# Optimization experiments

Measured on AMD Instinct MI355X. Metric: run time of the kernel, lower is better.

Reference implementation:

```python
import jax, jax.numpy as jnp
import numpy as np

N_NODES = 100000
N_EDGES = 1600000
HIDDEN = 128
N_GRAPHS = 64
N_CLASSES = 10


def setup_inputs() -> dict:
    key = jax.random.key(0)
    ks = jax.random.split(key, 10)
    x = jax.random.normal(ks[0], (N_NODES, 1), dtype=jnp.float32)
    edge_index = jax.random.randint(ks[1], (2, N_EDGES), 0, N_NODES, dtype=jnp.int32)
    batch = jnp.sort(jax.random.randint(ks[2], (N_NODES,), 0, N_GRAPHS, dtype=jnp.int32))
    def glorot(k, shape):
        fan_in, fan_out = shape
        s = jnp.sqrt(6.0 / (fan_in + fan_out))
        return jax.random.uniform(k, shape, jnp.float32, -s, s)
    return {
        "x": x,
        "edge_index": edge_index,
        "batch": batch,
        "W1l": glorot(ks[3], (1, HIDDEN)),
        "W1r": glorot(ks[4], (1, HIDDEN)),
        "b1": jnp.zeros((HIDDEN,), jnp.float32),
        "W2l": glorot(ks[5], (HIDDEN, HIDDEN)),
        "W2r": glorot(ks[6], (HIDDEN, HIDDEN)),
        "b2": jnp.zeros((HIDDEN,), jnp.float32),
        "W3l": glorot(ks[7], (HIDDEN, HIDDEN)),
        "W3r": glorot(ks[8], (HIDDEN, HIDDEN)),
        "b3": jnp.zeros((HIDDEN,), jnp.float32),
        "Wfc": glorot(ks[9], (HIDDEN, N_CLASSES)),
        "bfc": jnp.zeros((N_CLASSES,), jnp.float32),
    }


def _sage_conv(x, src, dst, Wl, Wr, b, n_nodes):
    # mean aggregation of source features at destination nodes
    msg = x[src]                                              # [E, d_in]
    agg = jax.ops.segment_sum(msg, dst, num_segments=n_nodes)  # [N, d_in]
    cnt = jax.ops.segment_sum(jnp.ones((src.shape[0], 1), x.dtype), dst,
                              num_segments=n_nodes)            # [N, 1]
    mean = agg / jnp.maximum(cnt, 1.0)
    # PyG SAGEConv: lin_l(mean neighbors) + bias + lin_r(self)
    return mean @ Wl + b + x @ Wr


def reference(x, edge_index, batch, W1l, W1r, b1, W2l, W2r, b2,
              W3l, W3r, b3, Wfc, bfc):
    src, dst = edge_index[0], edge_index[1]
    n = x.shape[0]
    h = jax.nn.relu(_sage_conv(x, src, dst, W1l, W1r, b1, n))
    h = jax.nn.relu(_sage_conv(h, src, dst, W2l, W2r, b2, n))
    h = jax.nn.relu(_sage_conv(h, src, dst, W3l, W3r, b3, n))
    # global_mean_pool over graph ids in `batch`
    pooled = jax.ops.segment_sum(h, batch, num_segments=N_GRAPHS)
    gcnt = jax.ops.segment_sum(jnp.ones((n, 1), h.dtype), batch,
                               num_segments=N_GRAPHS)
    pooled = pooled / jnp.maximum(gcnt, 1.0)
    logits = pooled @ Wfc + bfc
    return jax.nn.log_softmax(logits, axis=1)
```

## Files before the change

kernel.cpp:

```cpp
#include <hip/hip_runtime.h>

typedef unsigned int u32;
typedef unsigned short u16;
typedef short bf16x8 __attribute__((ext_vector_type(8)));
typedef float f32x4 __attribute__((ext_vector_type(4)));
typedef float f32x2 __attribute__((ext_vector_type(2)));
typedef u32 u32x4 __attribute__((ext_vector_type(4)));

#define HBLK 256

__device__ __forceinline__ u16 f2bf(float f) {
  u32 u = __float_as_uint(f);
  u = (u + 0x7FFFu + ((u >> 16) & 1u)) >> 16;
  return (u16)u;
}
__device__ __forceinline__ float bf2f(u32 h) { return __uint_as_float(h << 16); }

__global__ void hist_kernel(const int* __restrict__ dst, int* __restrict__ hist,
                            int E, int nbuk, int chunk) {
  __shared__ int h[1024];
  for (int i = threadIdx.x; i < nbuk; i += 256) h[i] = 0;
  __syncthreads();
  int b0 = blockIdx.x * chunk, b1 = min(b0 + chunk, E);
  for (int e = b0 + threadIdx.x; e < b1; e += 256)
    atomicAdd(&h[dst[e] >> 7], 1);
  __syncthreads();
  for (int i = threadIdx.x; i < nbuk; i += 256)
    hist[i * HBLK + blockIdx.x] = h[i];
}

__global__ void scan_local(const int* __restrict__ in, int* __restrict__ out,
                           int* __restrict__ bsum, int n) {
  __shared__ int s[256];
  int tid = threadIdx.x;
  int i = blockIdx.x * 256 + tid;
  int v = (i < n) ? in[i] : 0;
  s[tid] = v;
  __syncthreads();
  for (int off = 1; off < 256; off <<= 1) {
    int t = (tid >= off) ? s[tid - off] : 0;
    __syncthreads();
    s[tid] += t;
    __syncthreads();
  }
  if (i < n) out[i] = s[tid] - v;
  if (tid == 255) bsum[blockIdx.x] = s[255];
}

__global__ void scan_fix(int* __restrict__ a, const int* __restrict__ bsum, int n) {
  __shared__ int red[256];
  int tid = threadIdx.x, b = blockIdx.x;
  int s = 0;
  for (int k = tid; k < b; k += 256) s += bsum[k];
  red[tid] = s;
  __syncthreads();
  for (int off = 128; off; off >>= 1) {
    if (tid < off) red[tid] += red[tid + off];
    __syncthreads();
  }
  int i = b * 256 + tid;
  if (i < n) a[i] += red[0];
}

__global__ void scatter2_kernel(const int* __restrict__ src, const int* __restrict__ dst,
                                const int* __restrict__ hist_s, u32* __restrict__ part,
                                int E, int nbuk, int chunk) {
  __shared__ int cur[1024];
  for (int i = threadIdx.x; i < nbuk; i += 256)
    cur[i] = hist_s[i * HBLK + blockIdx.x];
  __syncthreads();
  int b0 = blockIdx.x * chunk, b1 = min(b0 + chunk, E);
  for (int e = b0 + threadIdx.x; e < b1; e += 256) {
    int d = dst[e];
    int pos = atomicAdd(&cur[d >> 7], 1);
    part[pos] = (u32)src[e] | ((u32)(d & 127) << 25);
  }
}

__global__ void scatter3_kernel(const u32* __restrict__ part, const int* __restrict__ hist_s,
                                const float* __restrict__ x,
                                int* __restrict__ roff, int* __restrict__ csr,
                                float* __restrict__ mean1, int E, int nbuk, int n) {
  int b = blockIdx.x;
  int tid = threadIdx.x;
  int base = hist_s[b * HBLK];
  int end = (b + 1 < nbuk) ? hist_s[(b + 1) * HBLK] : E;
  __shared__ int cnt[128];
  __shared__ int s[128];
  __shared__ int cur[128];
  __shared__ float xsum[128];
  if (tid < 128) { cnt[tid] = 0; xsum[tid] = 0.f; }
  __syncthreads();
  for (int e = base + tid; e < end; e += 256)
    atomicAdd(&cnt[part[e] >> 25], 1);
  __syncthreads();
  if (tid < 128) s[tid] = cnt[tid];
  __syncthreads();
  for (int off = 1; off < 128; off <<= 1) {
    int t = (tid >= off && tid < 128) ? s[tid - off] : 0;
    __syncthreads();
    if (tid < 128) s[tid] += t;
    __syncthreads();
  }
  if (tid < 128) {
    int excl = s[tid] - cnt[tid];
    cur[tid] = base + excl;
    int node = b * 128 + tid;
    if (node < n) roff[node] = base + excl;
  }
  if (b == 0 && tid == 0) roff[n] = E;
  __syncthreads();
  for (int e = base + tid; e < end; e += 256) {
    u32 p = part[e];
    int sidx = (int)(p & 0x1FFFFFFu);
    int pos = atomicAdd(&cur[p >> 25], 1);
    csr[pos] = sidx;
    atomicAdd(&xsum[p >> 25], x[sidx]);
  }
  __syncthreads();
  if (tid < 128) {
    int node = b * 128 + tid;
    if (node < n) mean1[node] = xsum[tid] / (float)max(cnt[tid], 1);
  }
}

__global__ void h1_kernel(const float* __restrict__ mean1, const float* __restrict__ x,
                          const float* __restrict__ W1l, const float* __restrict__ W1r,
                          const float* __restrict__ b1, u32* __restrict__ h1, int n) {
  int idx = blockIdx.x * 256 + threadIdx.x;
  if (idx >= n * 64) return;
  int i = idx >> 6, w = idx & 63;
  int j0 = w * 2;
  float m1 = mean1[i], xs = x[i];
  float v0 = fmaxf(m1 * W1l[j0] + xs * W1r[j0] + b1[j0], 0.f);
  float v1 = fmaxf(m1 * W1l[j0 + 1] + xs * W1r[j0 + 1] + b1[j0 + 1], 0.f);
  h1[idx] = (u32)f2bf(v0) | ((u32)f2bf(v1) << 16);
}

__global__ void wprep2_kernel(const float* __restrict__ W2l, const float* __restrict__ W2r,
                              const float* __restrict__ W3l, const float* __restrict__ W3r,
                              u16* __restrict__ wt2, u16* __restrict__ wt3,
                              float* __restrict__ pooled, int* __restrict__ gcnt) {
  int idx = blockIdx.x * 256 + threadIdx.x;
  int which = idx >> 15, r = idx & 32767;
  int j = r >> 8, k = r & 255;
  if (which == 0) {
    float v = (k < 128) ? W2l[k * 128 + j] : W2r[(k - 128) * 128 + j];
    wt2[r] = f2bf(v);
  } else {
    float v = (k < 128) ? W3l[k * 128 + j] : W3r[(k - 128) * 128 + j];
    wt3[r] = f2bf(v);
  }
  if (idx < 8192) pooled[idx] = 0.f;
  if (idx < 64) gcnt[idx] = 0;
}

__global__ void agg_kernel(const int* __restrict__ csr, const int* __restrict__ roff,
                           const u32* __restrict__ hin, u32* __restrict__ outv, int n) {
  int wave = threadIdx.x >> 6, lane = threadIdx.x & 63;
  int i = blockIdx.x * 4 + wave;
  if (i >= n) return;
  int grp = lane >> 4, li = lane & 15;
  int e0 = roff[i], e1 = roff[i + 1];
  f32x2 a[4] = {};
  int e = e0 + grp;
  for (; e + 12 < e1; e += 16) {
    int s0 = csr[e], s1 = csr[e + 4], s2 = csr[e + 8], s3 = csr[e + 12];
    u32x4 v0 = *(const u32x4*)(hin + (size_t)s0 * 64 + li * 4);
    u32x4 v1 = *(const u32x4*)(hin + (size_t)s1 * 64 + li * 4);
    u32x4 v2 = *(const u32x4*)(hin + (size_t)s2 * 64 + li * 4);
    u32x4 v3 = *(const u32x4*)(hin + (size_t)s3 * 64 + li * 4);
#pragma unroll
    for (int w = 0; w < 4; ++w) {
      a[w] += (f32x2){bf2f(v0[w] & 0xFFFFu), bf2f(v0[w] >> 16)};
      a[w] += (f32x2){bf2f(v1[w] & 0xFFFFu), bf2f(v1[w] >> 16)};
      a[w] += (f32x2){bf2f(v2[w] & 0xFFFFu), bf2f(v2[w] >> 16)};
      a[w] += (f32x2){bf2f(v3[w] & 0xFFFFu), bf2f(v3[w] >> 16)};
    }
  }
  for (; e + 4 < e1; e += 8) {
    int s0 = csr[e], s1 = csr[e + 4];
    u32x4 v0 = *(const u32x4*)(hin + (size_t)s0 * 64 + li * 4);
    u32x4 v1 = *(const u32x4*)(hin + (size_t)s1 * 64 + li * 4);
#pragma unroll
    for (int w = 0; w < 4; ++w) {
      a[w] += (f32x2){bf2f(v0[w] & 0xFFFFu), bf2f(v0[w] >> 16)};
      a[w] += (f32x2){bf2f(v1[w] & 0xFFFFu), bf2f(v1[w] >> 16)};
    }
  }
  if (e < e1) {
    int s0 = csr[e];
    u32x4 v0 = *(const u32x4*)(hin + (size_t)s0 * 64 + li * 4);
#pragma unroll
    for (int w = 0; w < 4; ++w)
      a[w] += (f32x2){bf2f(v0[w] & 0xFFFFu), bf2f(v0[w] >> 16)};
  }
#pragma unroll
  for (int w = 0; w < 4; ++w) {
    a[w].x += __shfl_xor(a[w].x, 16, 64);
    a[w].y += __shfl_xor(a[w].y, 16, 64);
    a[w].x += __shfl_xor(a[w].x, 32, 64);
    a[w].y += __shfl_xor(a[w].y, 32, 64);
  }
  if (grp == 0) {
    float inv = 1.f / (float)max(e1 - e0, 1);
    u32x4 o;
#pragma unroll
    for (int w = 0; w < 4; ++w)
      o[w] = (u32)f2bf(a[w].x * inv) | ((u32)f2bf(a[w].y * inv) << 16);
    *(u32x4*)(outv + (size_t)i * 64 + li * 4) = o;
  }
}

__launch_bounds__(512)
__global__ void mm_kernel(const u16* Aleft, const u16* Aright,
                          const u16* __restrict__ Wt, const float* __restrict__ bias,
                          u16* Out, int n) {
  __shared__ u16 wlds[32768];
  for (int c = threadIdx.x; c < 4096; c += 512) {
    int j = c >> 5, ch = c & 31;
    int swz = ch ^ (j & 31);
    *(u32x4*)(&wlds[j * 256 + swz * 8]) = *(const u32x4*)(&Wt[j * 256 + ch * 8]);
  }
  __syncthreads();
  int wave = threadIdx.x >> 6;
  int lane = threadIdx.x & 63;
  int quad = lane >> 4, l16 = lane & 15;
  int row0 = blockIdx.x * 128 + wave * 16;
  int m = row0 + l16;
  int mc = m < n ? m : (n - 1);
  f32x4 acc[8] = {};
  const u16* Ah[2] = {Aleft, Aright};
#pragma unroll
  for (int half = 0; half < 2; ++half) {
    const u16* A = Ah[half] + (size_t)mc * 128;
#pragma unroll
    for (int s = 0; s < 4; ++s) {
      bf16x8 a = *(const bf16x8*)(A + s * 32 + quad * 8);
      int chunk = (half << 4) + (s << 2) + quad;
#pragma unroll
      for (int t = 0; t < 8; ++t) {
        int j = t * 16 + l16;
        int swz = chunk ^ (j & 31);
        bf16x8 b = *(const bf16x8*)(&wlds[j * 256 + swz * 8]);
        acc[t] = __builtin_amdgcn_mfma_f32_16x16x32_bf16(a, b, acc[t], 0, 0, 0);
      }
    }
  }
#pragma unroll
  for (int t = 0; t < 8; ++t) {
    int j = t * 16 + l16;
    float bj = bias[j];
#pragma unroll
    for (int r = 0; r < 4; ++r) {
      int mr = row0 + quad * 4 + r;
      if (mr < n) {
        float v = acc[t][r] + bj;
        Out[(size_t)mr * 128 + j] = f2bf(fmaxf(v, 0.f));
      }
    }
  }
}

#define PB_NODES 256
__global__ void pool_partial(const int* __restrict__ batch, const u32* __restrict__ h3,
                             float* __restrict__ pooled, int* __restrict__ gcnt, int n) {
  int wave = threadIdx.x >> 6, lane = threadIdx.x & 63;
  int start = blockIdx.x * PB_NODES;
  int end = min(start + PB_NODES, n);
  float a0 = 0.f, a1 = 0.f;
  int gcur = -1, cnt = 0;
  for (int i = start + wave; i < end; i += 4) {
    int g = batch[i];
    if (g != gcur) {
      if (gcur >= 0) {
        atomicAdd(&pooled[gcur * 128 + lane * 2], a0);
        atomicAdd(&pooled[gcur * 128 + lane * 2 + 1], a1);
        if (lane == 0) atomicAdd(&gcnt[gcur], cnt);
      }
      gcur = g; a0 = 0.f; a1 = 0.f; cnt = 0;
    }
    u32 v = h3[(size_t)i * 64 + lane];
    a0 += bf2f(v & 0xFFFFu);
    a1 += bf2f(v >> 16);
    cnt++;
  }
  if (gcur >= 0) {
    atomicAdd(&pooled[gcur * 128 + lane * 2], a0);
    atomicAdd(&pooled[gcur * 128 + lane * 2 + 1], a1);
    if (lane == 0) atomicAdd(&gcnt[gcur], cnt);
  }
}

__global__ void head_kernel(const float* __restrict__ pooled, const int* __restrict__ gcnt,
                            const float* __restrict__ Wfc, const float* __restrict__ bfc,
                            float* __restrict__ out) {
  __shared__ float lg[64][10];
  int t = threadIdx.x;
  if (t < 640) {
    int g = t / 10, c = t % 10;
    float inv = 1.f / (float)max(gcnt[g], 1);
    float acc = bfc[c];
    for (int k = 0; k < 128; ++k) acc += pooled[g * 128 + k] * inv * Wfc[k * 10 + c];
    lg[g][c] = acc;
  }
  __syncthreads();
  if (t < 640) {
    int g = t / 10, c = t % 10;
    float mx = -1e30f;
    for (int q = 0; q < 10; ++q) mx = fmaxf(mx, lg[g][q]);
    float se = 0.f;
    for (int q = 0; q < 10; ++q) se += expf(lg[g][q] - mx);
    out[g * 10 + c] = lg[g][c] - mx - logf(se);
  }
}

extern "C" void kernel_launch(void* const* d_in, const int* in_sizes, int n_in,
                              void* d_out, int out_size, void* d_ws, size_t ws_size,
                              hipStream_t stream) {
  const float* x   = (const float*)d_in[0];
  const int* ei    = (const int*)d_in[1];
  const int* batch = (const int*)d_in[2];
  const float* W1l = (const float*)d_in[3];
  const float* W1r = (const float*)d_in[4];
  const float* b1  = (const float*)d_in[5];
  const float* W2l = (const float*)d_in[6];
  const float* W2r = (const float*)d_in[7];
  const float* b2  = (const float*)d_in[8];
  const float* W3l = (const float*)d_in[9];
  const float* W3r = (const float*)d_in[10];
  const float* b3  = (const float*)d_in[11];
  const float* Wfc = (const float*)d_in[12];
  const float* bfc = (const float*)d_in[13];
  float* out = (float*)d_out;
  int N = in_sizes[0];
  int E = in_sizes[1] / 2;
  const int* src = ei;
  const int* dst = ei + E;

  char* p = (char*)d_ws;
  auto alloc = [&](size_t bytes) { void* r = (void*)p; p += (bytes + 255) & ~(size_t)255; return r; };
  int* roff   = (int*)alloc((size_t)(N + 1) * 4);
  int* csr    = (int*)alloc((size_t)E * 4);
  float* mean1 = (float*)alloc((size_t)N * 4);
  u32* bufA   = (u32*)alloc((size_t)N * 64 * 4);
  u32* bufB   = (u32*)alloc((size_t)N * 64 * 4);
  u16* wt2    = (u16*)alloc(32768 * 2);
  u16* wt3    = (u16*)alloc(32768 * 2);
  float* pooled = (float*)alloc(64 * 128 * 4);
  int* gcnt   = (int*)alloc(64 * 4);
  int* bsum   = (int*)alloc(1024 * 4);

  int nbuk = (N + 127) >> 7;
  int* hist = (int*)bufA;
  u32* part = (u32*)bufB;
  int chunk = (E + HBLK - 1) / HBLK;
  int nH = nbuk * HBLK;
  int nbH = (nH + 255) / 256;

  hist_kernel<<<HBLK, 256, 0, stream>>>(dst, hist, E, nbuk, chunk);
  scan_local<<<nbH, 256, 0, stream>>>(hist, hist, bsum, nH);
  scan_fix<<<nbH, 256, 0, stream>>>(hist, bsum, nH);
  scatter2_kernel<<<HBLK, 256, 0, stream>>>(src, dst, hist, part, E, nbuk, chunk);
  scatter3_kernel<<<nbuk, 256, 0, stream>>>(part, hist, x, roff, csr, mean1, E, nbuk, N);
  wprep2_kernel<<<256, 256, 0, stream>>>(W2l, W2r, W3l, W3r, wt2, wt3, pooled, gcnt);
  h1_kernel<<<((size_t)N * 64 + 255) / 256, 256, 0, stream>>>(mean1, x, W1l, W1r, b1, bufA, N);
  agg_kernel<<<(N + 3) / 4, 256, 0, stream>>>(csr, roff, bufA, bufB, N);
  mm_kernel<<<(N + 127) / 128, 512, 0, stream>>>((const u16*)bufB, (const u16*)bufA, wt2, b2, (u16*)bufB, N);
  agg_kernel<<<(N + 3) / 4, 256, 0, stream>>>(csr, roff, bufB, bufA, N);
  mm_kernel<<<(N + 127) / 128, 512, 0, stream>>>((const u16*)bufA, (const u16*)bufB, wt3, b3, (u16*)bufA, N);
  pool_partial<<<(N + PB_NODES - 1) / PB_NODES, 256, 0, stream>>>(batch, bufA, pooled, gcnt, N);
  head_kernel<<<1, 640, 0, stream>>>(pooled, gcnt, Wfc, bfc, out);
}
```

Baseline: 368.0 us.

## Fuse weight prep into histogram, layer-1 into scatter3, and head into pooling

Weight transposition and zero-initialisation move into the histogram kernel. The layer-1 linear+ReLU moves into scatter3 using a per-block mean kept in shared memory, which removes the mean1 buffer and the separate h1 launch; a new bbase array is needed so scatter3 no longer reads the histogram that h1 now overwrites. The classifier head runs inside the pooling kernel through a last-block-done atomic counter. This cuts three kernel launches and one global round-trip, at the cost of a threadfence/atomic finish pattern and fewer threads writing h1.

```diff
diff --git a/kernel.cpp b/kernel.cpp
--- a/kernel.cpp
+++ b/kernel.cpp
@@ -16,8 +16,28 @@
 }
 __device__ __forceinline__ float bf2f(u32 h) { return __uint_as_float(h << 16); }
 
-__global__ void hist_kernel(const int* __restrict__ dst, int* __restrict__ hist,
-                            int E, int nbuk, int chunk) {
+__global__ void hist_wprep_kernel(const int* __restrict__ dst, int* __restrict__ hist,
+                                  int E, int nbuk, int chunk,
+                                  const float* __restrict__ W2l, const float* __restrict__ W2r,
+                                  const float* __restrict__ W3l, const float* __restrict__ W3r,
+                                  u16* __restrict__ wt2, u16* __restrict__ wt3,
+                                  float* __restrict__ pooled, int* __restrict__ gcnt,
+                                  int* __restrict__ done) {
+  int idx = blockIdx.x * 256 + threadIdx.x;
+  {
+    int which = idx >> 15, r = idx & 32767;
+    int j = r >> 8, k = r & 255;
+    if (which == 0) {
+      float v = (k < 128) ? W2l[k * 128 + j] : W2r[(k - 128) * 128 + j];
+      wt2[r] = f2bf(v);
+    } else {
+      float v = (k < 128) ? W3l[k * 128 + j] : W3r[(k - 128) * 128 + j];
+      wt3[r] = f2bf(v);
+    }
+    if (idx < 8192) pooled[idx] = 0.f;
+    if (idx < 64) gcnt[idx] = 0;
+    if (idx == 0) *done = 0;
+  }
   __shared__ int h[1024];
   for (int i = threadIdx.x; i < nbuk; i += 256) h[i] = 0;
   __syncthreads();
@@ -47,7 +67,8 @@
   if (tid == 255) bsum[blockIdx.x] = s[255];
 }
 
-__global__ void scan_fix(int* __restrict__ a, const int* __restrict__ bsum, int n) {
+__global__ void scan_fix(int* __restrict__ a, const int* __restrict__ bsum, int n,
+                         int* __restrict__ bbase) {
   __shared__ int red[256];
   int tid = threadIdx.x, b = blockIdx.x;
   int s = 0;
@@ -59,7 +80,11 @@
     __syncthreads();
   }
   int i = b * 256 + tid;
-  if (i < n) a[i] += red[0];
+  if (i < n) {
+    int v = a[i] + red[0];
+    a[i] = v;
+    if (tid == 0) bbase[b] = v;
+  }
 }
 
 __global__ void scatter2_kernel(const int* __restrict__ src, const int* __restrict__ dst,
@@ -77,19 +102,26 @@
   }
 }
 
-__global__ void scatter3_kernel(const u32* __restrict__ part, const int* __restrict__ hist_s,
+__global__ void scatter3_kernel(const u32* __restrict__ part, const int* __restrict__ bbase,
                                 const float* __restrict__ x,
+                                const float* __restrict__ W1l, const float* __restrict__ W1r,
+                                const float* __restrict__ b1,
                                 int* __restrict__ roff, int* __restrict__ csr,
-                                float* __restrict__ mean1, int E, int nbuk, int n) {
+                                u32* __restrict__ h1, int E, int nbuk, int n) {
   int b = blockIdx.x;
   int tid = threadIdx.x;
-  int base = hist_s[b * HBLK];
-  int end = (b + 1 < nbuk) ? hist_s[(b + 1) * HBLK] : E;
+  int base = bbase[b];
+  int end = (b + 1 < nbuk) ? bbase[b + 1] : E;
   __shared__ int cnt[128];
   __shared__ int s[128];
   __shared__ int cur[128];
   __shared__ float xsum[128];
-  if (tid < 128) { cnt[tid] = 0; xsum[tid] = 0.f; }
+  __shared__ float meanv[128];
+  __shared__ float wlA[128], wrA[128], bA[128];
+  if (tid < 128) {
+    cnt[tid] = 0; xsum[tid] = 0.f;
+    wlA[tid] = W1l[tid]; wrA[tid] = W1r[tid]; bA[tid] = b1[tid];
+  }
   __syncthreads();
   for (int e = base + tid; e < end; e += 256)
     atomicAdd(&cnt[part[e] >> 25], 1);
@@ -118,41 +150,18 @@
     atomicAdd(&xsum[p >> 25], x[sidx]);
   }
   __syncthreads();
-  if (tid < 128) {
-    int node = b * 128 + tid;
-    if (node < n) mean1[node] = xsum[tid] / (float)max(cnt[tid], 1);
-  }
-}
-
-__global__ void h1_kernel(const float* __restrict__ mean1, const float* __restrict__ x,
-                          const float* __restrict__ W1l, const float* __restrict__ W1r,
-                          const float* __restrict__ b1, u32* __restrict__ h1, int n) {
-  int idx = blockIdx.x * 256 + threadIdx.x;
-  if (idx >= n * 64) return;
-  int i = idx >> 6, w = idx & 63;
-  int j0 = w * 2;
-  float m1 = mean1[i], xs = x[i];
-  float v0 = fmaxf(m1 * W1l[j0] + xs * W1r[j0] + b1[j0], 0.f);
-  float v1 = fmaxf(m1 * W1l[j0 + 1] + xs * W1r[j0 + 1] + b1[j0 + 1], 0.f);
-  h1[idx] = (u32)f2bf(v0) | ((u32)f2bf(v1) << 16);
-}
-
-__global__ void wprep2_kernel(const float* __restrict__ W2l, const float* __restrict__ W2r,
-                              const float* __restrict__ W3l, const float* __restrict__ W3r,
-                              u16* __restrict__ wt2, u16* __restrict__ wt3,
-                              float* __restrict__ pooled, int* __restrict__ gcnt) {
-  int idx = blockIdx.x * 256 + threadIdx.x;
-  int which = idx >> 15, r = idx & 32767;
-  int j = r >> 8, k = r & 255;
-  if (which == 0) {
-    float v = (k < 128) ? W2l[k * 128 + j] : W2r[(k - 128) * 128 + j];
-    wt2[r] = f2bf(v);
-  } else {
-    float v = (k < 128) ? W3l[k * 128 + j] : W3r[(k - 128) * 128 + j];
-    wt3[r] = f2bf(v);
-  }
-  if (idx < 8192) pooled[idx] = 0.f;
-  if (idx < 64) gcnt[idx] = 0;
+  if (tid < 128) meanv[tid] = xsum[tid] / (float)max(cnt[tid], 1);
+  __syncthreads();
+  int nlocal = min(128, n - b * 128);
+  for (int q = tid; q < nlocal * 64; q += 256) {
+    int ln = q >> 6, w = q & 63;
+    int node = b * 128 + ln;
+    int j0 = w * 2;
+    float m = meanv[ln], xs = x[node];
+    float v0 = fmaxf(m * wlA[j0] + xs * wrA[j0] + bA[j0], 0.f);
+    float v1 = fmaxf(m * wlA[j0 + 1] + xs * wrA[j0 + 1] + bA[j0 + 1], 0.f);
+    h1[(size_t)node * 64 + w] = (u32)f2bf(v0) | ((u32)f2bf(v1) << 16);
+  }
 }
 
 __global__ void agg_kernel(const int* __restrict__ csr, const int* __restrict__ roff,
@@ -263,8 +272,10 @@
 }
 
 #define PB_NODES 256
-__global__ void pool_partial(const int* __restrict__ batch, const u32* __restrict__ h3,
-                             float* __restrict__ pooled, int* __restrict__ gcnt, int n) {
+__global__ void pool_head_kernel(const int* __restrict__ batch, const u32* __restrict__ h3,
+                                 float* __restrict__ pooled, int* __restrict__ gcnt,
+                                 const float* __restrict__ Wfc, const float* __restrict__ bfc,
+                                 float* __restrict__ out, int* __restrict__ done, int n) {
   int wave = threadIdx.x >> 6, lane = threadIdx.x & 63;
   int start = blockIdx.x * PB_NODES;
   int end = min(start + PB_NODES, n);
@@ -290,22 +301,28 @@
     atomicAdd(&pooled[gcur * 128 + lane * 2 + 1], a1);
     if (lane == 0) atomicAdd(&gcnt[gcur], cnt);
   }
-}
-
-__global__ void head_kernel(const float* __restrict__ pooled, const int* __restrict__ gcnt,
-                            const float* __restrict__ Wfc, const float* __restrict__ bfc,
-                            float* __restrict__ out) {
+  __threadfence();
+  __shared__ int amLast;
+  if (threadIdx.x == 0) amLast = (atomicAdd(done, 1) == (int)gridDim.x - 1);
+  __syncthreads();
+  if (!amLast) return;
+  __threadfence();
+  __shared__ float pl[8192];
+  __shared__ int gcs[64];
   __shared__ float lg[64][10];
-  int t = threadIdx.x;
-  if (t < 640) {
+  for (int idx = threadIdx.x; idx < 8192; idx += 256)
+    pl[idx] = atomicAdd(&pooled[idx], 0.0f);
+  if (threadIdx.x < 64) gcs[threadIdx.x] = atomicAdd(&gcnt[threadIdx.x], 0);
+  __syncthreads();
+  for (int t = threadIdx.x; t < 640; t += 256) {
     int g = t / 10, c = t % 10;
-    float inv = 1.f / (float)max(gcnt[g], 1);
+    float inv = 1.f / (float)max(gcs[g], 1);
     float acc = bfc[c];
-    for (int k = 0; k < 128; ++k) acc += pooled[g * 128 + k] * inv * Wfc[k * 10 + c];
+    for (int k = 0; k < 128; ++k) acc += pl[g * 128 + k] * inv * Wfc[k * 10 + c];
     lg[g][c] = acc;
   }
   __syncthreads();
-  if (t < 640) {
+  for (int t = threadIdx.x; t < 640; t += 256) {
     int g = t / 10, c = t % 10;
     float mx = -1e30f;
     for (int q = 0; q < 10; ++q) mx = fmaxf(mx, lg[g][q]);
@@ -342,7 +359,6 @@
   auto alloc = [&](size_t bytes) { void* r = (void*)p; p += (bytes + 255) & ~(size_t)255; return r; };
   int* roff   = (int*)alloc((size_t)(N + 1) * 4);
   int* csr    = (int*)alloc((size_t)E * 4);
-  float* mean1 = (float*)alloc((size_t)N * 4);
   u32* bufA   = (u32*)alloc((size_t)N * 64 * 4);
   u32* bufB   = (u32*)alloc((size_t)N * 64 * 4);
   u16* wt2    = (u16*)alloc(32768 * 2);
@@ -350,6 +366,8 @@
   float* pooled = (float*)alloc(64 * 128 * 4);
   int* gcnt   = (int*)alloc(64 * 4);
   int* bsum   = (int*)alloc(1024 * 4);
+  int* bbase  = (int*)alloc(1024 * 4);
+  int* done   = (int*)alloc(256);
 
   int nbuk = (N + 127) >> 7;
   int* hist = (int*)bufA;
@@ -358,17 +376,18 @@
   int nH = nbuk * HBLK;
   int nbH = (nH + 255) / 256;
 
-  hist_kernel<<<HBLK, 256, 0, stream>>>(dst, hist, E, nbuk, chunk);
+  hist_wprep_kernel<<<HBLK, 256, 0, stream>>>(dst, hist, E, nbuk, chunk,
+                                              W2l, W2r, W3l, W3r, wt2, wt3,
+                                              pooled, gcnt, done);
   scan_local<<<nbH, 256, 0, stream>>>(hist, hist, bsum, nH);
-  scan_fix<<<nbH, 256, 0, stream>>>(hist, bsum, nH);
+  scan_fix<<<nbH, 256, 0, stream>>>(hist, bsum, nH, bbase);
   scatter2_kernel<<<HBLK, 256, 0, stream>>>(src, dst, hist, part, E, nbuk, chunk);
-  scatter3_kernel<<<nbuk, 256, 0, stream>>>(part, hist, x, roff, csr, mean1, E, nbuk, N);
-  wprep2_kernel<<<256, 256, 0, stream>>>(W2l, W2r, W3l, W3r, wt2, wt3, pooled, gcnt);
-  h1_kernel<<<((size_t)N * 64 + 255) / 256, 256, 0, stream>>>(mean1, x, W1l, W1r, b1, bufA, N);
+  scatter3_kernel<<<nbuk, 256, 0, stream>>>(part, bbase, x, W1l, W1r, b1,
+                                            roff, csr, bufA, E, nbuk, N);
   agg_kernel<<<(N + 3) / 4, 256, 0, stream>>>(csr, roff, bufA, bufB, N);
   mm_kernel<<<(N + 127) / 128, 512, 0, stream>>>((const u16*)bufB, (const u16*)bufA, wt2, b2, (u16*)bufB, N);
   agg_kernel<<<(N + 3) / 4, 256, 0, stream>>>(csr, roff, bufB, bufA, N);
   mm_kernel<<<(N + 127) / 128, 512, 0, stream>>>((const u16*)bufA, (const u16*)bufB, wt3, b3, (u16*)bufA, N);
-  pool_partial<<<(N + PB_NODES - 1) / PB_NODES, 256, 0, stream>>>(batch, bufA, pooled, gcnt, N);
-  head_kernel<<<1, 640, 0, stream>>>(pooled, gcnt, Wfc, bfc, out);
-}
+  pool_head_kernel<<<(N + PB_NODES - 1) / PB_NODES, 256, 0, stream>>>(batch, bufA, pooled, gcnt,
+                                                                      Wfc, bfc, out, done, N);
+}
```

Result: slower. 384.9 us (+4.6%).
